# Optimization experiments

Measured on AMD Instinct MI355X. Metric: run time of the kernel, lower is better.

## Reference

```python
import jax, jax.numpy as jnp
import numpy as np

B, T, I, H, O = 8192, 180, 7, 64, 16

def setup_inputs() -> dict:
    key = jax.random.key(0)
    ks = jax.random.split(key, 8)
    s_ih = 1.0 / np.sqrt(H)
    x = jax.random.normal(ks[0], (B, T, I), dtype=jnp.float32)
    # PyTorch nn.LSTM param layout: [4H, in] with gate order i, f, g, o
    W_ih = jax.random.uniform(ks[1], (4 * H, I), jnp.float32, -s_ih, s_ih)
    W_hh = jax.random.uniform(ks[2], (4 * H, H), jnp.float32, -s_ih, s_ih)
    b_ih = jax.random.uniform(ks[3], (4 * H,), jnp.float32, -s_ih, s_ih)
    b_hh = jax.random.uniform(ks[4], (4 * H,), jnp.float32, -s_ih, s_ih)
    W_fc = jax.random.uniform(ks[5], (O, H), jnp.float32, -s_ih, s_ih)
    b_fc = jax.random.uniform(ks[6], (O,), jnp.float32, -s_ih, s_ih)
    return {"x": x, "W_ih": W_ih, "W_hh": W_hh, "b_ih": b_ih,
            "b_hh": b_hh, "W_fc": W_fc, "b_fc": b_fc}

def reference(x, W_ih, W_hh, b_ih, b_hh, W_fc, b_fc):
    x = x.reshape(-1, T, I)
    b = b_ih + b_hh
    # precompute input projections for all timesteps: [T, B, 4H]
    xg = jnp.einsum('bti,gi->tbg', x, W_ih) + b

    def step(carry, xg_t):
        h, c = carry
        gates = xg_t + h @ W_hh.T  # [B, 4H]
        i_g, f_g, g_g, o_g = jnp.split(gates, 4, axis=-1)
        i_g = jax.nn.sigmoid(i_g)
        f_g = jax.nn.sigmoid(f_g)
        g_g = jnp.tanh(g_g)
        o_g = jax.nn.sigmoid(o_g)
        c = f_g * c + i_g * g_g
        h = o_g * jnp.tanh(c)
        return (h, c), None

    h0 = jnp.zeros((x.shape[0], H), dtype=x.dtype)
    c0 = jnp.zeros((x.shape[0], H), dtype=x.dtype)
    (h_last, _), _ = jax.lax.scan(step, (h0, c0), xg)
    return h_last @ W_fc.T + b_fc  # [B, O]
```

## Files before the change

### kernel.cpp

```cpp
#include <hip/hip_runtime.h>
#include <math.h>

#ifndef __has_builtin
#define __has_builtin(x) 0
#endif

#if __has_builtin(__builtin_amdgcn_rcpf)
#define FAST_RCP(x) __builtin_amdgcn_rcpf(x)
#else
#define FAST_RCP(x) (1.0f / (x))
#endif

#if __has_builtin(__builtin_amdgcn_exp2f)
#define FAST_EXP2(x) __builtin_amdgcn_exp2f(x)
#else
#define FAST_EXP2(x) exp2f(x)
#endif

typedef _Float16 half8 __attribute__((ext_vector_type(8)));
typedef float f32x4 __attribute__((ext_vector_type(4)));

constexpr int T_STEPS  = 180;
constexpr int I_DIM    = 7;
constexpr int HDIM     = 64;
constexpr int BT       = 16;
constexpr int BSTRIDE  = 104;

__global__ __launch_bounds__(1024, 8) void lstm_mfma_kernel(
    const float* __restrict__ x,
    const float* __restrict__ W_ih,
    const float* __restrict__ W_hh,
    const float* __restrict__ b_ih,
    const float* __restrict__ b_hh,
    const float* __restrict__ W_fc,
    const float* __restrict__ b_fc,
    float* __restrict__ out) {
    __shared__ alignas(16) _Float16 Blds[2][BT][BSTRIDE];
    __shared__ float hlds[BT][HDIM + 4];

    const int tid  = (int)threadIdx.x;
    const int w    = tid >> 6;
    const int lane = tid & 63;
    const int q    = lane >> 4;
    const int n15  = lane & 15;
    const long bbase = (long)blockIdx.x * BT;

    half8 afrag[3];
    {
        const int unit = 4 * w + (n15 >> 2);
        const int gate = n15 & 3;
        const int grow = gate * HDIM + unit;
        const float scl = (gate == 2) ? 2.88539008177792681472f
                                      : -1.44269504088896340736f;
#pragma unroll
        for (int kc = 0; kc < 3; ++kc) {
#pragma unroll
            for (int j = 0; j < 8; ++j) {
                const int k = kc * 32 + q * 8 + j;
                float v;
                if (k < I_DIM)            v = W_ih[grow * I_DIM + k];
                else if (k == I_DIM)      v = b_ih[grow] + b_hh[grow];
                else if (k < 8 + HDIM)    v = W_hh[grow * HDIM + (k - 8)];
                else                      v = 0.0f;
                afrag[kc][j] = (_Float16)(scl * v);
            }
        }
    }

    for (int idx = tid; idx < 2 * BT * BSTRIDE; idx += 1024) {
        const int buf = idx / (BT * BSTRIDE);
        const int rem = idx % (BT * BSTRIDE);
        const int n = rem / BSTRIDE, k = rem % BSTRIDE;
        float v = 0.0f;
        if (k == I_DIM)                 v = 1.0f;
        else if (k < I_DIM && buf == 0) v = x[(bbase + n) * (T_STEPS * I_DIM) + k];
        Blds[buf][n][k] = (_Float16)v;
    }
    __syncthreads();

    const int ucell = 4 * w + q;

    const _Float16* const rb0 = &Blds[0][n15][q * 8];
    const _Float16* const rb1 = &Blds[1][n15][q * 8];
    _Float16* const hw0 = &Blds[0][n15][8 + ucell];
    _Float16* const hw1 = &Blds[1][n15][8 + ucell];

    const int xn = tid >> 3, xi = tid & 7;
    const bool xact = (tid < 128) && (xi < I_DIM);
    const float* const xcol = x + (bbase + xn) * (T_STEPS * I_DIM) + xi;
    _Float16* const xw0 = &Blds[0][xn][xi];
    _Float16* const xw1 = &Blds[1][xn][xi];

    float xA = xact ? xcol[1 * I_DIM] : 0.0f;
    float xB = xact ? xcol[2 * I_DIM] : 0.0f;

    float c = 0.0f, h = 0.0f;

#define LSTM_STEP(TT, RB, HW, XW, XREG)                                        \
    {                                                                          \
        const half8 bf0 = *(const half8*)(RB);                                 \
        const half8 bf1 = *(const half8*)((RB) + 32);                          \
        const half8 bf2 = *(const half8*)((RB) + 64);                          \
        if (xact && ((TT) + 1 < T_STEPS)) *(XW) = (_Float16)XREG;              \
        {                                                                      \
            int tl = (TT) + 3;                                                 \
            if (tl >= T_STEPS) tl = T_STEPS - 1;                               \
            if (xact) XREG = xcol[tl * I_DIM];                                 \
        }                                                                      \
        f32x4 acc = {0.f, 0.f, 0.f, 0.f};                                      \
        acc = __builtin_amdgcn_mfma_f32_16x16x32_f16(afrag[0], bf0, acc, 0, 0, 0); \
        acc = __builtin_amdgcn_mfma_f32_16x16x32_f16(afrag[1], bf1, acc, 0, 0, 0); \
        acc = __builtin_amdgcn_mfma_f32_16x16x32_f16(afrag[2], bf2, acc, 0, 0, 0); \
        const float A = FAST_EXP2(acc[0]);                                     \
        const float F = FAST_EXP2(acc[1]);                                     \
        const float E = FAST_EXP2(acc[2]);                                     \
        const float O = FAST_EXP2(acc[3]);                                     \
        const float ig = (E - 1.0f) * FAST_RCP((1.0f + A) * (E + 1.0f));       \
        const float fv = FAST_RCP(1.0f + F);                                   \
        c = fv * c + ig;                                                       \
        float cs = 2.88539008177792681472f * c;                                \
        cs = fminf(fmaxf(cs, -80.0f), 80.0f);                                  \
        const float C = FAST_EXP2(cs);                                         \
        h = (C - 1.0f) * FAST_RCP((1.0f + O) * (C + 1.0f));                    \
        *(HW) = (_Float16)h;                                                   \
        __syncthreads();                                                       \
    }

    for (int t = 0; t < T_STEPS; t += 2) {
        LSTM_STEP(t, rb0, hw1, xw1, xA)
        LSTM_STEP(t + 1, rb1, hw0, xw0, xB)
    }
#undef LSTM_STEP

    hlds[n15][ucell] = h;
    __syncthreads();
    if (tid < 256) {
        const int b = tid >> 4, j = tid & 15;
        float s = b_fc[j];
#pragma unroll 8
        for (int u = 0; u < HDIM; ++u)
            s += hlds[b][u] * W_fc[j * HDIM + u];
        out[(bbase + b) * 16 + j] = s;
    }
}

extern "C" void kernel_launch(void* const* d_in, const int* in_sizes, int n_in,
                              void* d_out, int out_size, void* d_ws, size_t ws_size,
                              hipStream_t stream) {
    const float* x    = (const float*)d_in[0];
    const float* W_ih = (const float*)d_in[1];
    const float* W_hh = (const float*)d_in[2];
    const float* b_ih = (const float*)d_in[3];
    const float* b_hh = (const float*)d_in[4];
    const float* W_fc = (const float*)d_in[5];
    const float* b_fc = (const float*)d_in[6];
    float* out = (float*)d_out;

    const int B = in_sizes[0] / (T_STEPS * I_DIM);
    const int grid = B / BT;

    lstm_mfma_kernel<<<grid, 1024, 0, stream>>>(x, W_ih, W_hh, b_ih, b_hh,
                                                W_fc, b_fc, out);
}
```

Before: 204.3 us.

## Halve block size by giving each wave two row tiles of LSTM gates

Each block now runs 8 waves (512 threads) instead of 16, and each wave computes two 16-row gate tiles with interleaved MFMA chains and two cell-state updates. Fewer waves per block should make the per-timestep __syncthreads barrier cheaper and give each wave more independent work to hide MFMA and transcendental latency. In exchange each wave holds more registers, and the per-step critical path per wave grows to two cell updates.

```diff
diff --git a/kernel.cpp b/kernel.cpp
--- a/kernel.cpp
+++ b/kernel.cpp
@@ -26,7 +26,7 @@
 constexpr int BT       = 16;
 constexpr int BSTRIDE  = 104;
 
-__global__ __launch_bounds__(1024, 8) void lstm_mfma_kernel(
+__global__ __launch_bounds__(512, 4) void lstm_mfma_kernel(
     const float* __restrict__ x,
     const float* __restrict__ W_ih,
     const float* __restrict__ W_hh,
@@ -45,9 +45,11 @@
     const int n15  = lane & 15;
     const long bbase = (long)blockIdx.x * BT;
 
-    half8 afrag[3];
-    {
-        const int unit = 4 * w + (n15 >> 2);
+    half8 afrag[2][3];
+#pragma unroll
+    for (int pt = 0; pt < 2; ++pt) {
+        const int rt   = 2 * w + pt;
+        const int unit = 4 * rt + (n15 >> 2);
         const int gate = n15 & 3;
         const int grow = gate * HDIM + unit;
         const float scl = (gate == 2) ? 2.88539008177792681472f
@@ -62,12 +64,12 @@
                 else if (k == I_DIM)      v = b_ih[grow] + b_hh[grow];
                 else if (k < 8 + HDIM)    v = W_hh[grow * HDIM + (k - 8)];
                 else                      v = 0.0f;
-                afrag[kc][j] = (_Float16)(scl * v);
+                afrag[pt][kc][j] = (_Float16)(scl * v);
             }
         }
     }
 
-    for (int idx = tid; idx < 2 * BT * BSTRIDE; idx += 1024) {
+    for (int idx = tid; idx < 2 * BT * BSTRIDE; idx += 512) {
         const int buf = idx / (BT * BSTRIDE);
         const int rem = idx % (BT * BSTRIDE);
         const int n = rem / BSTRIDE, k = rem % BSTRIDE;
@@ -78,12 +80,15 @@
     }
     __syncthreads();
 
-    const int ucell = 4 * w + q;
+    const int u0 = 8 * w + q;
+    const int u1 = u0 + 4;
 
     const _Float16* const rb0 = &Blds[0][n15][q * 8];
     const _Float16* const rb1 = &Blds[1][n15][q * 8];
-    _Float16* const hw0 = &Blds[0][n15][8 + ucell];
-    _Float16* const hw1 = &Blds[1][n15][8 + ucell];
+    _Float16* const h0w0 = &Blds[0][n15][8 + u0];
+    _Float16* const h1w0 = &Blds[0][n15][8 + u1];
+    _Float16* const h0w1 = &Blds[1][n15][8 + u0];
+    _Float16* const h1w1 = &Blds[1][n15][8 + u1];
 
     const int xn = tid >> 3, xi = tid & 7;
     const bool xact = (tid < 128) && (xi < I_DIM);
@@ -94,9 +99,24 @@
     float xA = xact ? xcol[1 * I_DIM] : 0.0f;
     float xB = xact ? xcol[2 * I_DIM] : 0.0f;
 
-    float c = 0.0f, h = 0.0f;
+    float c0 = 0.0f, c1 = 0.0f, h0 = 0.0f, h1 = 0.0f;
 
-#define LSTM_STEP(TT, RB, HW, XW, XREG)                                        \
+#define LSTM_CELL(ACC, CREG, HREG)                                             \
+    {                                                                          \
+        const float A = FAST_EXP2(ACC[0]);                                     \
+        const float F = FAST_EXP2(ACC[1]);                                     \
+        const float E = FAST_EXP2(ACC[2]);                                     \
+        const float O = FAST_EXP2(ACC[3]);                                     \
+        const float ig = (E - 1.0f) * FAST_RCP((1.0f + A) * (E + 1.0f));       \
+        const float fv = FAST_RCP(1.0f + F);                                   \
+        CREG = fv * CREG + ig;                                                 \
+        float cs = 2.88539008177792681472f * CREG;                             \
+        cs = fminf(fmaxf(cs, -80.0f), 80.0f);                                  \
+        const float C = FAST_EXP2(cs);                                         \
+        HREG = (C - 1.0f) * FAST_RCP((1.0f + O) * (C + 1.0f));                 \
+    }
+
+#define LSTM_STEP(TT, RB, HW0, HW1, XW, XREG)                                  \
     {                                                                          \
         const half8 bf0 = *(const half8*)(RB);                                 \
         const half8 bf1 = *(const half8*)((RB) + 32);                          \
@@ -107,32 +127,30 @@
             if (tl >= T_STEPS) tl = T_STEPS - 1;                               \
             if (xact) XREG = xcol[tl * I_DIM];                                 \
         }                                                                      \
-        f32x4 acc = {0.f, 0.f, 0.f, 0.f};                                      \
-        acc = __builtin_amdgcn_mfma_f32_16x16x32_f16(afrag[0], bf0, acc, 0, 0, 0); \
-        acc = __builtin_amdgcn_mfma_f32_16x16x32_f16(afrag[1], bf1, acc, 0, 0, 0); \
-        acc = __builtin_amdgcn_mfma_f32_16x16x32_f16(afrag[2], bf2, acc, 0, 0, 0); \
-        const float A = FAST_EXP2(acc[0]);                                     \
-        const float F = FAST_EXP2(acc[1]);                                     \
-        const float E = FAST_EXP2(acc[2]);                                     \
-        const float O = FAST_EXP2(acc[3]);                                     \
-        const float ig = (E - 1.0f) * FAST_RCP((1.0f + A) * (E + 1.0f));       \
-        const float fv = FAST_RCP(1.0f + F);                                   \
-        c = fv * c + ig;                                                       \
-        float cs = 2.88539008177792681472f * c;                                \
-        cs = fminf(fmaxf(cs, -80.0f), 80.0f);                                  \
-        const float C = FAST_EXP2(cs);                                         \
-        h = (C - 1.0f) * FAST_RCP((1.0f + O) * (C + 1.0f));                    \
-        *(HW) = (_Float16)h;                                                   \
+        f32x4 acc0 = {0.f, 0.f, 0.f, 0.f};                                     \
+        f32x4 acc1 = {0.f, 0.f, 0.f, 0.f};                                     \
+        acc0 = __builtin_amdgcn_mfma_f32_16x16x32_f16(afrag[0][0], bf0, acc0, 0, 0, 0); \
+        acc1 = __builtin_amdgcn_mfma_f32_16x16x32_f16(afrag[1][0], bf0, acc1, 0, 0, 0); \
+        acc0 = __builtin_amdgcn_mfma_f32_16x16x32_f16(afrag[0][1], bf1, acc0, 0, 0, 0); \
+        acc1 = __builtin_amdgcn_mfma_f32_16x16x32_f16(afrag[1][1], bf1, acc1, 0, 0, 0); \
+        acc0 = __builtin_amdgcn_mfma_f32_16x16x32_f16(afrag[0][2], bf2, acc0, 0, 0, 0); \
+        acc1 = __builtin_amdgcn_mfma_f32_16x16x32_f16(afrag[1][2], bf2, acc1, 0, 0, 0); \
+        LSTM_CELL(acc0, c0, h0)                                                \
+        LSTM_CELL(acc1, c1, h1)                                                \
+        *(HW0) = (_Float16)h0;                                                 \
+        *(HW1) = (_Float16)h1;                                                 \
         __syncthreads();                                                       \
     }
 
     for (int t = 0; t < T_STEPS; t += 2) {
-        LSTM_STEP(t, rb0, hw1, xw1, xA)
-        LSTM_STEP(t + 1, rb1, hw0, xw0, xB)
+        LSTM_STEP(t, rb0, h0w1, h1w1, xw1, xA)
+        LSTM_STEP(t + 1, rb1, h0w0, h1w0, xw0, xB)
     }
 #undef LSTM_STEP
+#undef LSTM_CELL
 
-    hlds[n15][ucell] = h;
+    hlds[n15][u0] = h0;
+    hlds[n15][u1] = h1;
     __syncthreads();
     if (tid < 256) {
         const int b = tid >> 4, j = tid & 15;
@@ -159,6 +177,6 @@
     const int B = in_sizes[0] / (T_STEPS * I_DIM);
     const int grid = B / BT;
 
-    lstm_mfma_kernel<<<grid, 1024, 0, stream>>>(x, W_ih, W_hh, b_ih, b_hh,
-                                                W_fc, b_fc, out);
+    lstm_mfma_kernel<<<grid, 512, 0, stream>>>(x, W_ih, W_hh, b_ih, b_hh,
+                                               W_fc, b_fc, out);
 }
```

Result: no change. 201.2 us (-1.5%).
